# Kernel optimization log

Measured on AMD Instinct MI355X. Metric: run time of the kernel, lower is better.

Reference implementation:

```python
import jax, jax.numpy as jnp
import numpy as np


def _compute_features(ff):
    # ff: (..., 4) = [rx, ry, rvx, rvy]
    rx, ry, rvx, rvy = ff[..., 0], ff[..., 1], ff[..., 2], ff[..., 3]
    dist_sq = rx * rx + ry * ry
    dist = jnp.sqrt(dist_sq + 1e-06)
    inv_dist = 1.0 / (dist + 0.1)
    dir_x = rx / (dist + 1e-06)
    dir_y = ry / (dist + 1e-06)
    speed_sq = rvx * rvx + rvy * rvy
    rel_speed = jnp.sqrt(speed_sq + 1e-06)
    dot_vp = rvx * rx + rvy * ry
    closing_speed = dot_vp / (dist + 1e-06)
    ttca = jnp.tanh(-dot_vp / (speed_sq + 1e-06))
    return jnp.stack(
        [rx, ry, rvx, rvy, dist, inv_dist, rel_speed, closing_speed,
         dir_x, dir_y, ttca, dot_vp], axis=-1)  # (..., 12)


def setup_inputs() -> dict:
    key = jax.random.key(0)
    k0, k1, k2, k3, k4 = jax.random.split(key, 5)
    B, N, H, HID, IN = 16, 256, 8, 64, 12
    ff = jax.random.normal(k0, (B, N, N, 4), dtype=jnp.float32)
    # nn.Linear default init scale ~ 1/sqrt(fan_in); use small random weights
    W1 = jax.random.normal(k1, (IN, HID), dtype=jnp.float32) / np.sqrt(IN)
    b1 = jax.random.normal(k2, (HID,), dtype=jnp.float32) / np.sqrt(IN)
    W2 = jax.random.normal(k3, (HID, H), dtype=jnp.float32) / np.sqrt(HID)
    b2 = jax.random.normal(k4, (H,), dtype=jnp.float32) / np.sqrt(HID)
    return {"fundamental_features": ff, "W1": W1, "b1": b1, "W2": W2, "b2": b2}


def reference(fundamental_features, W1, b1, W2, b2):
    feats = _compute_features(fundamental_features)          # (B, N, N, 12)
    h = jax.nn.silu(jnp.einsum('bnmf,fh->bnmh', feats, W1) + b1)  # (B, N, N, 64)
    bias = jnp.einsum('bnmh,ho->bnmo', h, W2) + b2            # (B, N, N, H)
    return jnp.transpose(bias, (0, 3, 1, 2))                  # (B, H, N, N)
```

## Files before the change

### kernel.cpp

```cpp
#include <hip/hip_runtime.h>
#include <hip/hip_bf16.h>

#define NH 8
#define HID 64
#define NPAIRS (16 * 256 * 256)
#define BLOCK 256
#define LROW 72

typedef __attribute__((ext_vector_type(8))) short bf16x8;
typedef __attribute__((ext_vector_type(4))) float f32x4;
typedef __attribute__((ext_vector_type(16))) float f32x16;

union F8 { bf16x8 v; unsigned u[4]; uint4 q4; };

__device__ inline unsigned pk2(float a, float b) {
    __hip_bfloat162 h = __float22bfloat162_rn(make_float2(a, b));
    unsigned u;
    __builtin_memcpy(&u, &h, 4);
    return u;
}

__global__ void pack_weights(const float* __restrict__ W1, const float* __restrict__ b1,
                             const float* __restrict__ W2, const float* __restrict__ b2,
                             unsigned char* __restrict__ ws) {
    int l = threadIdx.x;
    int n32 = l & 31, q2 = l >> 5;
    int n16 = l & 15, q4 = l >> 4;
    unsigned* B1 = (unsigned*)ws;
    unsigned* B2 = (unsigned*)(ws + 2048);
    float* b2v = (float*)(ws + 4096);
    for (int m = 0; m < 2; ++m) {
        int h = m * 32 + n32;
        for (int j2 = 0; j2 < 4; ++j2) {
            int k0 = q2 * 8 + 2 * j2, k1 = k0 + 1;
            float v0 = (k0 < 12) ? W1[k0 * HID + h] : (k0 == 12 ? b1[h] : 0.f);
            float v1 = (k1 < 12) ? W1[k1 * HID + h] : 0.f;
            B1[(m * 64 + l) * 4 + j2] = pk2(v0, v1);
        }
    }
    for (int kc = 0; kc < 2; ++kc)
        for (int j2 = 0; j2 < 4; ++j2) {
            int k0 = kc * 32 + q4 * 8 + 2 * j2;
            float v0 = (n16 < NH) ? W2[k0 * NH + n16] : 0.f;
            float v1 = (n16 < NH) ? W2[(k0 + 1) * NH + n16] : 0.f;
            B2[(kc * 64 + l) * 4 + j2] = pk2(v0, v1);
        }
    b2v[l] = (n16 < NH) ? b2[n16] : 0.f;
}

__global__ __launch_bounds__(BLOCK) void relfeat_mfma3(
    const float* __restrict__ ff, const unsigned char* __restrict__ ws,
    float* __restrict__ out)
{
    __shared__ unsigned short lds[4][32 * LROW];
    const int tid = threadIdx.x;
    const int w = tid >> 6, l = tid & 63;
    const int n32 = l & 31, q2 = l >> 5;
    const int n16 = l & 15, q4 = l >> 4;
    unsigned short* my = lds[w];

    F8 B1f[2], B2f[2];
    B1f[0].q4 = ((const uint4*)ws)[l];
    B1f[1].q4 = ((const uint4*)ws)[64 + l];
    B2f[0].q4 = ((const uint4*)(ws + 2048))[l];
    B2f[1].q4 = ((const uint4*)(ws + 2048))[64 + l];
    const float b2s = ((const float*)(ws + 4096))[l];

    f32x16 z16;
    #pragma unroll
    for (int r = 0; r < 16; ++r) z16[r] = 0.f;

    const int wave_base = (blockIdx.x * 4 + w) * 128;

    #pragma unroll
    for (int it = 0; it < 2; ++it) {
        const int pbase = wave_base + it * 64;

        float4 v = ((const float4*)ff)[pbase + l];
        float rx = v.x, ry = v.y, rvx = v.z, rvy = v.w;
        float dist = sqrtf(rx * rx + ry * ry + 1e-6f);
        float speed_sq = rvx * rvx + rvy * rvy;
        float dot_vp = rvx * rx + rvy * ry;
        float invd = __builtin_amdgcn_rcpf(dist + 1e-6f);
        float inv_dist = __builtin_amdgcn_rcpf(dist + 0.1f);
        float rel_speed = sqrtf(speed_sq + 1e-6f);
        float closing = dot_vp * invd;
        float dir_x = rx * invd, dir_y = ry * invd;
        float zz = -dot_vp * __builtin_amdgcn_rcpf(speed_sq + 1e-6f);
        float ez = __expf(2.f * zz);
        float ttca = 1.f - 2.f * __builtin_amdgcn_rcpf(ez + 1.f);

        unsigned c0 = pk2(rx, ry), c1 = pk2(rvx, rvy);
        unsigned c2 = pk2(dist, inv_dist), c3 = pk2(rel_speed, closing);
        unsigned c4 = pk2(dir_x, dir_y), c5 = pk2(ttca, dot_vp);
        unsigned sw0 = (unsigned)__shfl_xor((int)c0, 32);
        unsigned sw1 = (unsigned)__shfl_xor((int)c1, 32);
        unsigned sw2 = (unsigned)__shfl_xor((int)c2, 32);
        unsigned sw3 = (unsigned)__shfl_xor((int)c3, 32);
        unsigned sw4 = (unsigned)__shfl_xor((int)c4, 32);
        unsigned sw5 = (unsigned)__shfl_xor((int)c5, 32);

        const bool hi = (q2 != 0);
        F8 frag[2];
        frag[0].u[0] = hi ? sw4 : c0;
        frag[0].u[1] = hi ? sw5 : c1;
        frag[0].u[2] = hi ? 0x00003f80u : c2;
        frag[0].u[3] = hi ? 0u : c3;
        frag[1].u[0] = hi ? c4 : sw0;
        frag[1].u[1] = hi ? c5 : sw1;
        frag[1].u[2] = hi ? 0x00003f80u : sw2;
        frag[1].u[3] = hi ? 0u : sw3;

        #pragma unroll
        for (int G = 0; G < 2; ++G) {
            const int pg = pbase + G * 32;

            #pragma unroll
            for (int m = 0; m < 2; ++m) {
                f32x16 d1 = __builtin_amdgcn_mfma_f32_32x32x16_bf16(frag[G].v, B1f[m].v, z16, 0, 0, 0);
                #pragma unroll
                for (int r = 0; r < 16; ++r) {
                    int prow = (r & 3) + 8 * (r >> 2) + 4 * q2;
                    float x = d1[r];
                    float s = x * __builtin_amdgcn_rcpf(1.f + __expf(-x));
                    my[prow * LROW + m * 32 + n32] = (unsigned short)pk2(s, s);
                }
            }

            #pragma unroll
            for (int hl = 0; hl < 2; ++hl) {
                f32x4 d2 = {b2s, b2s, b2s, b2s};
                #pragma unroll
                for (int kc = 0; kc < 2; ++kc) {
                    F8 a2;
                    a2.q4 = *(const uint4*)((const unsigned char*)my
                              + (hl * 16 + n16) * (LROW * 2) + kc * 64 + q4 * 16);
                    d2 = __builtin_amdgcn_mfma_f32_16x16x32_bf16(a2.v, B2f[kc].v, d2, 0, 0, 0);
                }
                if (n16 < NH) {
                    int p0 = pg + hl * 16 + q4 * 4;
                    int b = p0 >> 16, lo16 = p0 & 65535;
                    float4 st; st.x = d2[0]; st.y = d2[1]; st.z = d2[2]; st.w = d2[3];
                    *(float4*)(out + (size_t)b * (NH * 65536) + (size_t)n16 * 65536 + lo16) = st;
                }
            }
        }
    }
}

extern "C" void kernel_launch(void* const* d_in, const int* in_sizes, int n_in,
                              void* d_out, int out_size, void* d_ws, size_t ws_size,
                              hipStream_t stream) {
    const float* ff = (const float*)d_in[0];
    const float* W1 = (const float*)d_in[1];
    const float* b1 = (const float*)d_in[2];
    const float* W2 = (const float*)d_in[3];
    const float* b2 = (const float*)d_in[4];
    float* out = (float*)d_out;
    unsigned char* ws = (unsigned char*)d_ws;

    pack_weights<<<1, 64, 0, stream>>>(W1, b1, W2, b2, ws);
    const int grid = NPAIRS / (128 * 4);
    relfeat_mfma3<<<grid, BLOCK, 0, stream>>>(ff, ws, out);
}
```

Measured before the change: 102.4 us.

## Fuse weight packing into main kernel and transpose first MFMA for vectorized LDS stores

Removes the separate single-block pack_weights launch and has every wave build its bf16 weight fragments directly from global W1/b1/W2/b2. The first-layer MFMA operands are swapped so each lane holds four consecutive hidden units for one pair, which allows packed 8-byte LDS stores instead of 16 scalar 2-byte stores. Both ff loads are issued up front to overlap with weight loading, and launch bounds now request 4 blocks per CU. The cost is redundant scalar weight loads and conversions in every wave, plus possible register pressure from the occupancy hint.

```diff
diff --git a/kernel.cpp b/kernel.cpp
--- a/kernel.cpp
+++ b/kernel.cpp
@@ -20,36 +20,14 @@
     return u;
 }
 
-__global__ void pack_weights(const float* __restrict__ W1, const float* __restrict__ b1,
-                             const float* __restrict__ W2, const float* __restrict__ b2,
-                             unsigned char* __restrict__ ws) {
-    int l = threadIdx.x;
-    int n32 = l & 31, q2 = l >> 5;
-    int n16 = l & 15, q4 = l >> 4;
-    unsigned* B1 = (unsigned*)ws;
-    unsigned* B2 = (unsigned*)(ws + 2048);
-    float* b2v = (float*)(ws + 4096);
-    for (int m = 0; m < 2; ++m) {
-        int h = m * 32 + n32;
-        for (int j2 = 0; j2 < 4; ++j2) {
-            int k0 = q2 * 8 + 2 * j2, k1 = k0 + 1;
-            float v0 = (k0 < 12) ? W1[k0 * HID + h] : (k0 == 12 ? b1[h] : 0.f);
-            float v1 = (k1 < 12) ? W1[k1 * HID + h] : 0.f;
-            B1[(m * 64 + l) * 4 + j2] = pk2(v0, v1);
-        }
-    }
-    for (int kc = 0; kc < 2; ++kc)
-        for (int j2 = 0; j2 < 4; ++j2) {
-            int k0 = kc * 32 + q4 * 8 + 2 * j2;
-            float v0 = (n16 < NH) ? W2[k0 * NH + n16] : 0.f;
-            float v1 = (n16 < NH) ? W2[(k0 + 1) * NH + n16] : 0.f;
-            B2[(kc * 64 + l) * 4 + j2] = pk2(v0, v1);
-        }
-    b2v[l] = (n16 < NH) ? b2[n16] : 0.f;
+__device__ inline float silu(float x) {
+    return x * __builtin_amdgcn_rcpf(1.f + __expf(-x));
 }
 
-__global__ __launch_bounds__(BLOCK) void relfeat_mfma3(
-    const float* __restrict__ ff, const unsigned char* __restrict__ ws,
+__global__ __launch_bounds__(BLOCK, 4) void relfeat_mfma4(
+    const float* __restrict__ ff,
+    const float* __restrict__ W1, const float* __restrict__ b1,
+    const float* __restrict__ W2, const float* __restrict__ b2,
     float* __restrict__ out)
 {
     __shared__ unsigned short lds[4][32 * LROW];
@@ -59,24 +37,44 @@
     const int n16 = l & 15, q4 = l >> 4;
     unsigned short* my = lds[w];
 
+    const int wave_base = (blockIdx.x * 4 + w) * 128;
+
+    float4 va = ((const float4*)ff)[wave_base + l];
+    float4 vb = ((const float4*)ff)[wave_base + 64 + l];
+
     F8 B1f[2], B2f[2];
-    B1f[0].q4 = ((const uint4*)ws)[l];
-    B1f[1].q4 = ((const uint4*)ws)[64 + l];
-    B2f[0].q4 = ((const uint4*)(ws + 2048))[l];
-    B2f[1].q4 = ((const uint4*)(ws + 2048))[64 + l];
-    const float b2s = ((const float*)(ws + 4096))[l];
+    #pragma unroll
+    for (int m = 0; m < 2; ++m) {
+        int h = m * 32 + n32;
+        #pragma unroll
+        for (int j2 = 0; j2 < 4; ++j2) {
+            int k0 = q2 * 8 + 2 * j2, k1 = k0 + 1;
+            float v0 = (k0 < 12) ? W1[k0 * HID + h] : (k0 == 12 ? b1[h] : 0.f);
+            float v1 = (k1 < 12) ? W1[k1 * HID + h] : 0.f;
+            B1f[m].u[j2] = pk2(v0, v1);
+        }
+    }
+    #pragma unroll
+    for (int kc = 0; kc < 2; ++kc) {
+        #pragma unroll
+        for (int j2 = 0; j2 < 4; ++j2) {
+            int k0 = kc * 32 + q4 * 8 + 2 * j2;
+            float v0 = (n16 < NH) ? W2[k0 * NH + n16] : 0.f;
+            float v1 = (n16 < NH) ? W2[(k0 + 1) * NH + n16] : 0.f;
+            B2f[kc].u[j2] = pk2(v0, v1);
+        }
+    }
+    const float b2s = (n16 < NH) ? b2[n16] : 0.f;
 
     f32x16 z16;
     #pragma unroll
     for (int r = 0; r < 16; ++r) z16[r] = 0.f;
 
-    const int wave_base = (blockIdx.x * 4 + w) * 128;
-
     #pragma unroll
     for (int it = 0; it < 2; ++it) {
         const int pbase = wave_base + it * 64;
+        float4 v = it ? vb : va;
 
-        float4 v = ((const float4*)ff)[pbase + l];
         float rx = v.x, ry = v.y, rvx = v.z, rvy = v.w;
         float dist = sqrtf(rx * rx + ry * ry + 1e-6f);
         float speed_sq = rvx * rvx + rvy * rvy;
@@ -116,14 +114,19 @@
             const int pg = pbase + G * 32;
 
             #pragma unroll
-            for (int m = 0; m < 2; ++m) {
-                f32x16 d1 = __builtin_amdgcn_mfma_f32_32x32x16_bf16(frag[G].v, B1f[m].v, z16, 0, 0, 0);
+            for (int mh = 0; mh < 2; ++mh) {
+                f32x16 d1 = __builtin_amdgcn_mfma_f32_32x32x16_bf16(
+                                B1f[mh].v, frag[G].v, z16, 0, 0, 0);
                 #pragma unroll
-                for (int r = 0; r < 16; ++r) {
-                    int prow = (r & 3) + 8 * (r >> 2) + 4 * q2;
-                    float x = d1[r];
-                    float s = x * __builtin_amdgcn_rcpf(1.f + __expf(-x));
-                    my[prow * LROW + m * 32 + n32] = (unsigned short)pk2(s, s);
+                for (int t = 0; t < 4; ++t) {
+                    float s0 = silu(d1[4 * t + 0]);
+                    float s1 = silu(d1[4 * t + 1]);
+                    float s2 = silu(d1[4 * t + 2]);
+                    float s3 = silu(d1[4 * t + 3]);
+                    uint2 wv;
+                    wv.x = pk2(s0, s1);
+                    wv.y = pk2(s2, s3);
+                    *(uint2*)&my[n32 * LROW + mh * 32 + 8 * t + 4 * q2] = wv;
                 }
             }
 
@@ -157,9 +160,8 @@
     const float* W2 = (const float*)d_in[3];
     const float* b2 = (const float*)d_in[4];
     float* out = (float*)d_out;
-    unsigned char* ws = (unsigned char*)d_ws;
+    (void)d_ws; (void)ws_size;
 
-    pack_weights<<<1, 64, 0, stream>>>(W1, b1, W2, b2, ws);
     const int grid = NPAIRS / (128 * 4);
-    relfeat_mfma3<<<grid, BLOCK, 0, stream>>>(ff, ws, out);
+    relfeat_mfma4<<<grid, BLOCK, 0, stream>>>(ff, W1, b1, W2, b2, out);
 }
```

Result: no change. 101.3 us (-1.1%).
